# Kernel optimization log

Hardware: AMD Instinct MI355X
Metric: run time of the kernel (lower is better)

## Reference

```python
import jax, jax.numpy as jnp
import numpy as np

S = 2048      # sequence length (q_seq == kv_seq, self-attention)
D = 1024      # hidden_size
H = 16        # num_heads
DH = D // H   # per-head dim
LN_EPS = 1e-5


def setup_inputs() -> dict:
    key = jax.random.key(0)
    ks = jax.random.split(key, 8)
    init = lambda k, shape: (jax.random.normal(k, shape, dtype=jnp.float32)
                             / np.float32(np.sqrt(shape[-1])))
    return {
        "x": jax.random.normal(ks[0], (S, D), dtype=jnp.float32),
        "logit_bias": jax.random.normal(ks[1], (S, H * S), dtype=jnp.float32) * 0.1,
        "mask": jax.random.bernoulli(ks[2], 0.9, (S, S)),
        "Wq": init(ks[3], (D, D)),
        "Wk": init(ks[4], (D, D)),
        "Wv": init(ks[5], (D, D)),
        "Wo": init(ks[6], (D, D)),
        "ln_w": jnp.ones((D,), dtype=jnp.float32),
        "ln_b": jnp.zeros((D,), dtype=jnp.float32),
    }


def reference(x, logit_bias, mask, Wq, Wk, Wv, Wo, ln_w, ln_b):
    # Projections (eqx.nn.Linear: y = W @ x, no bias), split into heads.
    q = (x @ Wq.T).reshape(S, H, DH)  # [s,h,d]
    k = (x @ Wk.T).reshape(S, H, DH)  # [S,h,d]
    v = (x @ Wv.T).reshape(S, H, DH)  # [S,h,d]

    # Scaled scores + per-head additive logit bias.
    scale = jnp.asarray(1.0 / np.sqrt(DH), dtype=q.dtype)
    logits = jnp.einsum('shd,Shd->hsS', q * scale, k)  # [h,s,S]
    logits = logits + logit_bias.reshape(S, H, S).transpose(1, 0, 2)

    # Boolean mask (q_seq, kv_seq) broadcast over heads.
    logits = jnp.where(mask[None, :, :], logits, jnp.finfo(logits.dtype).min)

    # Stable softmax in float32 (matches result_type promotion in source).
    weights = jax.nn.softmax(logits.astype(jnp.float32), axis=-1).astype(logits.dtype)

    attn = jnp.einsum('hsS,Shd->shd', weights, v).reshape(S, D)
    attn_out = attn @ Wo.T  # output projection, no bias

    # Residual + LayerNorm over last dim (eqx.nn.LayerNorm, eps=1e-5).
    res = attn_out + x
    mean = jnp.mean(res, axis=-1, keepdims=True)
    var = jnp.var(res, axis=-1, keepdims=True)
    normed = (res - mean) * jax.lax.rsqrt(var + LN_EPS)
    return normed * ln_w + ln_b
```

## Files before the change

kernel.cpp:

```cpp
#include <hip/hip_runtime.h>

#define SS 2048
#define DD 1024
#define HH 16
#define DHD 64
#define HSN (HH * SS)
#define LOG2E 1.44269504088896340736f

typedef __bf16 bf16x8 __attribute__((ext_vector_type(8)));
typedef __bf16 bf16x4 __attribute__((ext_vector_type(4)));
typedef float f32x4 __attribute__((ext_vector_type(4)));
typedef unsigned int u32;
typedef unsigned long long u64;

__device__ __forceinline__ void glds16(const void* g, void* l) {
  __builtin_amdgcn_global_load_lds(
      (const __attribute__((address_space(1))) u32*)(const u32*)g,
      (__attribute__((address_space(3))) u32*)(u32*)l, 16, 0, 0);
}

__global__ __launch_bounds__(256) void cvt_all_kernel(const float* __restrict__ x,
                                                      const float* __restrict__ Wq,
                                                      const float* __restrict__ Wk,
                                                      const float* __restrict__ Wv,
                                                      const float* __restrict__ Wo,
                                                      __bf16* xb, __bf16* Wqb, __bf16* Wkb,
                                                      __bf16* Wvb, __bf16* Wob) {
  const int z = blockIdx.z;
  const int n4 = (z == 0 ? SS * DD : DD * DD) / 4;
  const int i = blockIdx.x * 256 + threadIdx.x;
  if (i >= n4) return;
  const float* in = z == 0 ? x : (z == 1 ? Wq : (z == 2 ? Wk : (z == 3 ? Wv : Wo)));
  __bf16* out = z == 0 ? xb : (z == 1 ? Wqb : (z == 2 ? Wkb : (z == 3 ? Wvb : Wob)));
  const float4 v = ((const float4*)in)[i];
  bf16x4 r;
  r[0] = (__bf16)v.x; r[1] = (__bf16)v.y; r[2] = (__bf16)v.z; r[3] = (__bf16)v.w;
  *(bf16x4*)&out[(long)i * 4] = r;
}

__global__ __launch_bounds__(256) void pack_mask(const int* __restrict__ mask,
                                                 u64* __restrict__ mp) {
  const long i = (long)blockIdx.x * 256 + threadIdx.x;
  const u64 b = __ballot(mask[i] != 0);
  if ((threadIdx.x & 63) == 0) mp[i >> 6] = b;
}

template <int BM>
__device__ __forceinline__ void gemm_body(const __bf16* __restrict__ A,
                                          const __bf16* __restrict__ B,
                                          void* __restrict__ Cout, float scale, int mode,
                                          int bx, int by) {
  constexpr int MR = BM / 32;
  __shared__ alignas(16) __bf16 As[BM * 32];
  __shared__ alignas(16) __bf16 Bs[128 * 32];
  const int tid = threadIdx.x;
  const int lane = tid & 63;
  const int wave = tid >> 6;
  const long m0 = (long)by * BM;
  const long n0 = (long)bx * 128;
  const int wm = (wave >> 1) * (BM / 2);
  const int wn = (wave & 1) * 64;
  const int g = lane >> 4, r16 = lane & 15;
  const int srow = tid >> 2, sseg = (tid & 3) * 8;

  f32x4 acc[MR][4] = {};

  for (int k0 = 0; k0 < DD; k0 += 32) {
#pragma unroll
    for (int it = 0; it < 2; ++it) {
      const int row = srow + it * 64;
      glds16(&B[(n0 + row) * DD + k0 + sseg], &Bs[row * 32 + sseg]);
    }
#pragma unroll
    for (int it = 0; it < BM / 64; ++it) {
      const int row = srow + it * 64;
      glds16(&A[(m0 + row) * DD + k0 + sseg], &As[row * 32 + sseg]);
    }
    __syncthreads();
    bf16x8 af[MR], bfr[4];
#pragma unroll
    for (int r = 0; r < MR; ++r) af[r] = *(const bf16x8*)&As[(wm + r * 16 + r16) * 32 + g * 8];
#pragma unroll
    for (int c = 0; c < 4; ++c) bfr[c] = *(const bf16x8*)&Bs[(wn + c * 16 + r16) * 32 + g * 8];
#pragma unroll
    for (int r = 0; r < MR; ++r)
#pragma unroll
      for (int c = 0; c < 4; ++c)
        acc[r][c] = __builtin_amdgcn_mfma_f32_16x16x32_bf16(af[r], bfr[c], acc[r][c], 0, 0, 0);
    __syncthreads();
  }

  if (mode == 2) {
#pragma unroll
    for (int r = 0; r < MR; ++r)
#pragma unroll
      for (int c = 0; c < 4; ++c) {
        const long row0 = m0 + wm + r * 16 + g * 4;
        const long col = n0 + wn + c * 16 + r16;
        bf16x4 rv;
#pragma unroll
        for (int i = 0; i < 4; ++i) rv[i] = (__bf16)(acc[r][c][i] * scale);
        *(bf16x4*)&((__bf16*)Cout)[col * SS + row0] = rv;
      }
  } else {
#pragma unroll
    for (int r = 0; r < MR; ++r)
#pragma unroll
      for (int c = 0; c < 4; ++c)
#pragma unroll
        for (int i = 0; i < 4; ++i) {
          const long row = m0 + wm + r * 16 + g * 4 + i;
          const long col = n0 + wn + c * 16 + r16;
          const float v = acc[r][c][i] * scale;
          if (mode == 1) ((float*)Cout)[row * DD + col] = v;
          else           ((__bf16*)Cout)[row * DD + col] = (__bf16)v;
        }
  }
}

__global__ __launch_bounds__(256) void gemm_qkv(const __bf16* __restrict__ A,
                                                const __bf16* __restrict__ B0,
                                                const __bf16* __restrict__ B1,
                                                const __bf16* __restrict__ B2,
                                                __bf16* C0, __bf16* C1, __bf16* C2,
                                                float s0) {
  const int z = blockIdx.z;
  const __bf16* B = z == 0 ? B0 : (z == 1 ? B1 : B2);
  __bf16* C = z == 0 ? C0 : (z == 1 ? C1 : C2);
  gemm_body<64>(A, B, C, z == 0 ? s0 : 1.0f, z == 2 ? 2 : 0, blockIdx.x, blockIdx.y);
}

__global__ __launch_bounds__(256) void gemm_o(const __bf16* __restrict__ A,
                                              const __bf16* __restrict__ B,
                                              float* __restrict__ C) {
  gemm_body<64>(A, B, C, 1.0f, 1, blockIdx.x, blockIdx.y);
}

__global__ __launch_bounds__(256) void attn_kernel(
    const __bf16* __restrict__ Q, const __bf16* __restrict__ K,
    const __bf16* __restrict__ Vt, const float* __restrict__ bias,
    const u64* __restrict__ mp, __bf16* __restrict__ Aout) {
  __shared__ alignas(16) __bf16 Ks[64][72];
  __shared__ alignas(16) __bf16 Vts[64][72];
  __shared__ alignas(16) __bf16 Ps[4][16][72];
  const int tid = threadIdx.x;
  const int lane = tid & 63;
  const int wave = tid >> 6;
  const int h = blockIdx.y;
  const int q0 = blockIdx.x * 64 + wave * 16;
  const int g = lane >> 4, r16 = lane & 15;
  const int myq = q0 + r16;
  const int srow = tid >> 2;

  bf16x8 qf[2];
#pragma unroll
  for (int c = 0; c < 2; ++c)
    qf[c] = *(const bf16x8*)&Q[(long)myq * DD + h * DHD + c * 32 + g * 8];

  const float* bp = &bias[(long)myq * HSN + h * SS];
  const u64* mrow_p = &mp[(long)myq * (SS / 64)];

  f32x4 o[4] = {};
  float mrow = -__builtin_inff();
  float lsum = 0.f;

  for (int kv0 = 0; kv0 < SS; kv0 += 64) {
    __syncthreads();
#pragma unroll
    for (int it = 0; it < 2; ++it) {
      const int seg = (tid & 3) + it * 4;
      *(bf16x8*)&Ks[srow][seg * 8] =
          *(const bf16x8*)&K[(long)(kv0 + srow) * DD + h * DHD + seg * 8];
      *(bf16x8*)&Vts[srow][seg * 8] =
          *(const bf16x8*)&Vt[(long)(h * DHD + srow) * SS + kv0 + seg * 8];
    }

    float4 bv[4];
#pragma unroll
    for (int t = 0; t < 4; ++t) bv[t] = *(const float4*)&bp[kv0 + t * 16 + g * 4];
    const u64 mw = mrow_p[kv0 >> 6];
    __syncthreads();

    f32x4 s[4];
#pragma unroll
    for (int t = 0; t < 4; ++t) {
      bf16x8 kf0 = *(const bf16x8*)&Ks[t * 16 + r16][g * 8];
      bf16x8 kf1 = *(const bf16x8*)&Ks[t * 16 + r16][32 + g * 8];
      f32x4 acc = {};
      acc = __builtin_amdgcn_mfma_f32_16x16x32_bf16(kf0, qf[0], acc, 0, 0, 0);
      s[t] = __builtin_amdgcn_mfma_f32_16x16x32_bf16(kf1, qf[1], acc, 0, 0, 0);
    }

    float sv[4][4];
#pragma unroll
    for (int t = 0; t < 4; ++t) {
      const u32 mb = (u32)(mw >> (t * 16 + g * 4));
      sv[t][0] = (mb & 1u) ? s[t][0] + bv[t].x * LOG2E : -1e38f;
      sv[t][1] = (mb & 2u) ? s[t][1] + bv[t].y * LOG2E : -1e38f;
      sv[t][2] = (mb & 4u) ? s[t][2] + bv[t].z * LOG2E : -1e38f;
      sv[t][3] = (mb & 8u) ? s[t][3] + bv[t].w * LOG2E : -1e38f;
    }

    float m4 = -1e38f;
#pragma unroll
    for (int t = 0; t < 4; ++t)
#pragma unroll
      for (int i = 0; i < 4; ++i) m4 = fmaxf(m4, sv[t][i]);
    m4 = fmaxf(m4, __shfl_xor(m4, 16));
    m4 = fmaxf(m4, __shfl_xor(m4, 32));
    const float mnew = fmaxf(mrow, m4);
    const float alpha = exp2f(mrow - mnew);
    float ps = 0.f;
    float p[4][4];
#pragma unroll
    for (int t = 0; t < 4; ++t)
#pragma unroll
      for (int i = 0; i < 4; ++i) {
        p[t][i] = exp2f(sv[t][i] - mnew);
        ps += p[t][i];
      }
    ps += __shfl_xor(ps, 16);
    ps += __shfl_xor(ps, 32);
    lsum = lsum * alpha + ps;
    mrow = mnew;
#pragma unroll
    for (int db = 0; db < 4; ++db) o[db] *= alpha;

#pragma unroll
    for (int t = 0; t < 4; ++t) {
      bf16x4 pb;
#pragma unroll
      for (int i = 0; i < 4; ++i) pb[i] = (__bf16)p[t][i];
      *(bf16x4*)&Ps[wave][r16][t * 16 + g * 4] = pb;
    }

#pragma unroll
    for (int kh = 0; kh < 2; ++kh) {
      bf16x8 pf = *(const bf16x8*)&Ps[wave][r16][kh * 32 + g * 8];
#pragma unroll
      for (int db = 0; db < 4; ++db) {
        bf16x8 vf = *(const bf16x8*)&Vts[db * 16 + r16][kh * 32 + g * 8];
        o[db] = __builtin_amdgcn_mfma_f32_16x16x32_bf16(vf, pf, o[db], 0, 0, 0);
      }
    }
  }

  const float rn = 1.f / lsum;
#pragma unroll
  for (int db = 0; db < 4; ++db) {
    bf16x4 r;
#pragma unroll
    for (int i = 0; i < 4; ++i) r[i] = (__bf16)(o[db][i] * rn);
    *(bf16x4*)&Aout[(long)myq * DD + h * DHD + db * 16 + g * 4] = r;
  }
}

__global__ __launch_bounds__(256) void ln_kernel(const float* __restrict__ attn_out,
                                                 const float* __restrict__ x,
                                                 const float* __restrict__ w,
                                                 const float* __restrict__ b,
                                                 float* __restrict__ out) {
  const long row = blockIdx.x;
  const int tid = threadIdx.x;
  const float4 a4 = ((const float4*)&attn_out[row * DD])[tid];
  const float4 x4 = ((const float4*)&x[row * DD])[tid];
  float v[4] = {a4.x + x4.x, a4.y + x4.y, a4.z + x4.z, a4.w + x4.w};
  float s = 0.f, s2 = 0.f;
#pragma unroll
  for (int j = 0; j < 4; ++j) { s += v[j]; s2 += v[j] * v[j]; }
#pragma unroll
  for (int off = 1; off < 64; off <<= 1) {
    s  += __shfl_xor(s, off);
    s2 += __shfl_xor(s2, off);
  }
  __shared__ float ss[4], ss2[4];
  if ((tid & 63) == 0) { ss[tid >> 6] = s; ss2[tid >> 6] = s2; }
  __syncthreads();
  s = ss[0] + ss[1] + ss[2] + ss[3];
  s2 = ss2[0] + ss2[1] + ss2[2] + ss2[3];
  const float mean = s * (1.f / DD);
  const float var = s2 * (1.f / DD) - mean * mean;
  const float inv = rsqrtf(var + 1e-5f);
  const float4 w4 = ((const float4*)w)[tid];
  const float4 b4 = ((const float4*)b)[tid];
  float4 o4;
  o4.x = (v[0] - mean) * inv * w4.x + b4.x;
  o4.y = (v[1] - mean) * inv * w4.y + b4.y;
  o4.z = (v[2] - mean) * inv * w4.z + b4.z;
  o4.w = (v[3] - mean) * inv * w4.w + b4.w;
  ((float4*)&out[row * DD])[tid] = o4;
}

extern "C" void kernel_launch(void* const* d_in, const int* in_sizes, int n_in,
                              void* d_out, int out_size, void* d_ws, size_t ws_size,
                              hipStream_t stream) {
  const float* x    = (const float*)d_in[0];
  const float* bias = (const float*)d_in[1];
  const int*   mask = (const int*)d_in[2];
  const float* Wq   = (const float*)d_in[3];
  const float* Wk   = (const float*)d_in[4];
  const float* Wv   = (const float*)d_in[5];
  const float* Wo   = (const float*)d_in[6];
  const float* lnw  = (const float*)d_in[7];
  const float* lnb  = (const float*)d_in[8];
  float* out = (float*)d_out;

  char* ws = (char*)d_ws;
  const size_t MB = 1024 * 1024;
  __bf16* xb   = (__bf16*)(ws + 0);
  __bf16* Wqb  = (__bf16*)(ws + 4 * MB);
  __bf16* Wkb  = (__bf16*)(ws + 6 * MB);
  __bf16* Wvb  = (__bf16*)(ws + 8 * MB);
  __bf16* Wob  = (__bf16*)(ws + 10 * MB);
  __bf16* Qb   = (__bf16*)(ws + 12 * MB);
  __bf16* Kb   = (__bf16*)(ws + 16 * MB);
  __bf16* Vtb  = (__bf16*)(ws + 24 * MB);
  __bf16* Atnb = (__bf16*)(ws + 28 * MB);
  float*  AOut = (float*)(ws + 32 * MB);
  u64*    mpk  = (u64*)(ws + 40 * MB);

  cvt_all_kernel<<<dim3(SS * DD / 1024, 1, 5), dim3(256), 0, stream>>>(
      x, Wq, Wk, Wv, Wo, xb, Wqb, Wkb, Wvb, Wob);

  pack_mask<<<dim3(SS * SS / 256), dim3(256), 0, stream>>>(mask, mpk);

  gemm_qkv<<<dim3(DD / 128, SS / 64, 3), dim3(256), 0, stream>>>(
      xb, Wqb, Wkb, Wvb, Qb, Kb, Vtb, 0.125f * LOG2E);

  attn_kernel<<<dim3(SS / 64, HH), dim3(256), 0, stream>>>(Qb, Kb, Vtb, bias, mpk, Atnb);

  gemm_o<<<dim3(DD / 128, SS / 64), dim3(256), 0, stream>>>(Atnb, Wob, AOut);

  ln_kernel<<<dim3(SS), dim3(256), 0, stream>>>(AOut, x, lnw, lnb, out);
}
```

Measured before the change: 487.4 us.

## Software-pipeline K/V and bias/mask loads one tile ahead in attention loop

```diff
diff --git a/kernel.cpp b/kernel.cpp
--- a/kernel.cpp
+++ b/kernel.cpp
@@ -164,21 +164,36 @@
   float mrow = -__builtin_inff();
   float lsum = 0.f;
 
-  for (int kv0 = 0; kv0 < SS; kv0 += 64) {
-    __syncthreads();
+  bf16x8 kreg[2], vreg[2];
+  float4 bvA[4], bvB[4];
+  u64 mwA, mwB;
+
+  auto loadKV = [&](int kv0) {
 #pragma unroll
     for (int it = 0; it < 2; ++it) {
       const int seg = (tid & 3) + it * 4;
-      *(bf16x8*)&Ks[srow][seg * 8] =
-          *(const bf16x8*)&K[(long)(kv0 + srow) * DD + h * DHD + seg * 8];
-      *(bf16x8*)&Vts[srow][seg * 8] =
-          *(const bf16x8*)&Vt[(long)(h * DHD + srow) * SS + kv0 + seg * 8];
-    }
-
-    float4 bv[4];
+      kreg[it] = *(const bf16x8*)&K[(long)(kv0 + srow) * DD + h * DHD + seg * 8];
+      vreg[it] = *(const bf16x8*)&Vt[(long)(h * DHD + srow) * SS + kv0 + seg * 8];
+    }
+  };
+  auto loadBM = [&](int kv0, float4 (&bv)[4], u64& mw) {
 #pragma unroll
     for (int t = 0; t < 4; ++t) bv[t] = *(const float4*)&bp[kv0 + t * 16 + g * 4];
-    const u64 mw = mrow_p[kv0 >> 6];
+    mw = mrow_p[kv0 >> 6];
+  };
+
+  auto tile = [&](int kvt, const float4 (&bvC)[4], u64 mwC,
+                  float4 (&bvN)[4], u64& mwN) {
+    __syncthreads();
+#pragma unroll
+    for (int it = 0; it < 2; ++it) {
+      const int seg8 = ((tid & 3) + it * 4) * 8;
+      *(bf16x8*)&Ks[srow][seg8] = kreg[it];
+      *(bf16x8*)&Vts[srow][seg8] = vreg[it];
+    }
+    const int kvn = (kvt + 64 < SS) ? kvt + 64 : 0;
+    loadKV(kvn);
+    loadBM(kvn, bvN, mwN);
     __syncthreads();
 
     f32x4 s[4];
@@ -194,11 +209,11 @@
     float sv[4][4];
 #pragma unroll
     for (int t = 0; t < 4; ++t) {
-      const u32 mb = (u32)(mw >> (t * 16 + g * 4));
-      sv[t][0] = (mb & 1u) ? s[t][0] + bv[t].x * LOG2E : -1e38f;
-      sv[t][1] = (mb & 2u) ? s[t][1] + bv[t].y * LOG2E : -1e38f;
-      sv[t][2] = (mb & 4u) ? s[t][2] + bv[t].z * LOG2E : -1e38f;
-      sv[t][3] = (mb & 8u) ? s[t][3] + bv[t].w * LOG2E : -1e38f;
+      const u32 mb = (u32)(mwC >> (t * 16 + g * 4));
+      sv[t][0] = (mb & 1u) ? s[t][0] + bvC[t].x * LOG2E : -1e38f;
+      sv[t][1] = (mb & 2u) ? s[t][1] + bvC[t].y * LOG2E : -1e38f;
+      sv[t][2] = (mb & 4u) ? s[t][2] + bvC[t].z * LOG2E : -1e38f;
+      sv[t][3] = (mb & 8u) ? s[t][3] + bvC[t].w * LOG2E : -1e38f;
     }
 
     float m4 = -1e38f;
@@ -243,6 +258,13 @@
         o[db] = __builtin_amdgcn_mfma_f32_16x16x32_bf16(vf, pf, o[db], 0, 0, 0);
       }
     }
+  };
+
+  loadKV(0);
+  loadBM(0, bvA, mwA);
+  for (int kv0 = 0; kv0 < SS; kv0 += 128) {
+    tile(kv0, bvA, mwA, bvB, mwB);
+    tile(kv0 + 64, bvB, mwB, bvA, mwA);
   }
 
   const float rn = 1.f / lsum;
```

After: 481.0 us. No clear change (-1.3%).
